# Performance work log

Hardware: AMD Instinct MI355X
Metric: run time of the kernel (lower is better)

## Reference

```python
import jax, jax.numpy as jnp
import numpy as np

B, T, C = 8, 1024, 1024
H, HS = 16, 64            # n_head, head_size
K, STRIDE = 32, 16        # block_length, stride_length
WIN = 128                 # local_window_size
EPS = 1e-5


def _ln(z, w):
    m = jnp.mean(z, axis=-1, keepdims=True)
    v = jnp.var(z, axis=-1, keepdims=True)
    return (z - m) / jnp.sqrt(v + EPS) * w


def setup_inputs() -> dict:
    key = jax.random.key(0)
    ks = jax.random.split(key, 8)
    s = 0.02
    return {
        "x": jax.random.normal(ks[0], (B, T, C), jnp.float32),
        "c_attn_w": jax.random.normal(ks[1], (3 * C, C), jnp.float32) * s,
        "conv_w": jax.random.normal(ks[2], (HS, HS, K), jnp.float32) * s,
        "ln_comp_w": jnp.ones((HS,), jnp.float32),
        "ln_local_w": jnp.ones((C,), jnp.float32),
        "gate_w1": jax.random.normal(ks[3], (C, 2 * C), jnp.float32) * s,
        "gate_ln_w": jnp.ones((C,), jnp.float32),
        "gate_w2": jax.random.normal(ks[4], (2, C), jnp.float32) * s,
        "c_proj_w": jax.random.normal(ks[5], (C, C), jnp.float32) * s,
    }


def reference(x, c_attn_w, conv_w, ln_comp_w, ln_local_w, gate_w1, gate_ln_w, gate_w2, c_proj_w):
    qkv = jnp.einsum('btc,oc->bto', x, c_attn_w)          # [B,T,3C]
    q, k, v = jnp.split(qkv, 3, axis=-1)
    def heads(t):
        return t.reshape(B, T, H, HS).transpose(0, 2, 1, 3)  # [B,H,T,hs]
    q, k, v = heads(q), heads(k), heads(v)

    # CompressionMLP: Conv1d over time + LayerNorm(hs) + exact GELU
    def compress(t):
        xr = t.transpose(0, 1, 3, 2).reshape(B * H, HS, T)   # [B*H, hs, T]
        co = jax.lax.conv_general_dilated(
            xr, conv_w, window_strides=(STRIDE,), padding='VALID',
            dimension_numbers=('NCH', 'OIH', 'NCH'))          # [B*H, hs, NB]
        co = co.transpose(0, 2, 1)                            # [B*H, NB, hs]
        co = jax.nn.gelu(_ln(co, ln_comp_w), approximate=False)
        nb = co.shape[1]
        return co.reshape(B, H, nb, HS)

    kc = compress(k)
    vc = compress(v)
    NB = kc.shape[2]  # 63
    scale = 1.0 / np.sqrt(HS)

    ti = jnp.arange(T)
    band = (ti[None, :] <= ti[:, None]) & (ti[None, :] >= ti[:, None] - WIN)  # [T,T]
    s_loc = jnp.einsum('bhqd,bhkd->bhqk', q, k) * scale
    s_loc = jnp.where(band[None, None], s_loc, -jnp.inf)
    local_out = jnp.einsum('bhqk,bhkd->bhqd', jax.nn.softmax(s_loc, axis=-1), v)
    local_out = local_out.transpose(0, 2, 1, 3).reshape(B, T, C)
    local_norm = _ln(local_out, ln_local_w)

    # compressed-KV attention with block-causal mask: block j <= token i
    bj = jnp.arange(NB)
    cmask = bj[None, :] <= ti[:, None]                        # [T,NB]
    s_cmp = jnp.einsum('bhqd,bhkd->bhqk', q, kc) * scale
    s_cmp = jnp.where(cmask[None, None], s_cmp, -jnp.inf)
    comp_out = jnp.einsum('bhqk,bhkd->bhqd', jax.nn.softmax(s_cmp, axis=-1), vc)
    comp_out = comp_out.transpose(0, 2, 1, 3).reshape(B, T, C)

    # AttentionGating: last-token features -> Linear -> LN -> ReLU -> Linear -> softmax
    feats = jnp.concatenate([local_norm[:, -1, :], comp_out[:, -1, :]], axis=-1)  # [B,2C]
    h = jax.nn.relu(_ln(feats @ gate_w1.T, gate_ln_w))
    gates = jax.nn.softmax(h @ gate_w2.T, axis=-1)            # [B,2]

    combined = gates[:, None, 0:1] * local_norm + gates[:, None, 1:2] * comp_out
    y = jnp.einsum('btc,oc->bto', combined, c_proj_w)
    return y
```

## Files before the change

### kernel.cpp

```cpp
#include <hip/hip_runtime.h>
#include <cstdint>
#include <cmath>
#include <cstddef>

typedef unsigned int u32;
typedef unsigned short u16;
typedef __bf16 bf16x8 __attribute__((ext_vector_type(8)));
typedef float f32x4 __attribute__((ext_vector_type(4)));
typedef u32 u32x4 __attribute__((ext_vector_type(4)));
typedef u32 u32x2 __attribute__((ext_vector_type(2)));

#define DEV static __device__ __forceinline__

DEV float bflo(u32 u) { return __uint_as_float(u << 16); }
DEV float bfhi(u32 u) { return __uint_as_float(u & 0xffff0000u); }
DEV u16 f2bf(float f) {
  u32 u = __float_as_uint(f);
  u += 0x7fffu + ((u >> 16) & 1u);
  return (u16)(u >> 16);
}
DEV f32x4 unpack_bf4(u32x2 r) {
  return (f32x4){bflo(r[0]), bfhi(r[0]), bflo(r[1]), bfhi(r[1])};
}
DEV float wredsum(float v) {
#pragma unroll
  for (int o = 32; o; o >>= 1) v += __shfl_xor(v, o, 64);
  return v;
}

DEV void gload_lds16(const u16* g, u16* lds_base) {
  __builtin_amdgcn_global_load_lds((const __attribute__((address_space(1))) void*)g,
                                   (__attribute__((address_space(3))) void*)lds_base,
                                   16, 0, 0);
}

__global__ __launch_bounds__(256) void fused_cast(const float* __restrict__ x,
                                                  const float* __restrict__ aw,
                                                  const float* __restrict__ pw,
                                                  const float* __restrict__ cw,
                                                  u16* __restrict__ xb,
                                                  u16* __restrict__ wab,
                                                  u16* __restrict__ wpb,
                                                  u16* __restrict__ wcb,
                                                  u16* __restrict__ kcb,
                                                  u16* __restrict__ vcb) {
  const int blk = blockIdx.x;
  if (blk < 12288) {
    const float* src;
    u16* dst;
    int base;
    if (blk < 8192) { src = x; dst = xb; base = blk; }
    else if (blk < 11264) { src = aw; dst = wab; base = blk - 8192; }
    else { src = pw; dst = wpb; base = blk - 11264; }
    const size_t idx = ((size_t)base * 256 + threadIdx.x) * 4;
    const f32x4 v = *(const f32x4*)&src[idx];
    u32x2 r;
    r[0] = (u32)f2bf(v[0]) | ((u32)f2bf(v[1]) << 16);
    r[1] = (u32)f2bf(v[2]) | ((u32)f2bf(v[3]) << 16);
    *(u32x2*)&dst[idx] = r;
  } else if (blk < 12800) {
    const int idx = (blk - 12288) * 256 + threadIdx.x;
    const int o = idx >> 11;
    const int rest = idx & 2047;
    const int i = rest >> 5;
    const int kk = rest & 31;
    wcb[(o << 11) + (kk << 6) + i] = f2bf(cw[idx]);
  } else {
    for (int i = threadIdx.x; i < 8192; i += 256) {
      const int bh = i >> 6, d = i & 63;
      kcb[bh * 4096 + 63 * 64 + d] = 0;
      vcb[bh * 4096 + d * 64 + 63] = 0;
    }
  }
}

template <int OUT_BF16>
__global__ __launch_bounds__(256, 4) void gemm_bt(const u16* __restrict__ A,
                                                  const u16* __restrict__ Bm,
                                                  void* __restrict__ out,
                                                  int M, int N, int K) {
  __shared__ u16 As[128 * 64];
  __shared__ u16 Bs[128 * 64];
  const int tid = threadIdx.x;
  const int lane = tid & 63;
  const int w = tid >> 6;
  const int row0 = blockIdx.x * 128;
  const int col0 = blockIdx.y * 128;
  const int wm = (w >> 1) * 64, wn = (w & 1) * 64;
  const int lr = lane & 15, lq = lane >> 4;
  const int srow = lane >> 3;
  const int scol = ((lane & 7) ^ (srow & 7)) * 8;
  const int pgA = ((lq ^ (lr & 7)) * 8);

  f32x4 acc[4][4] = {};

  for (int k0 = 0; k0 < K; k0 += 64) {
    __syncthreads();
#pragma unroll
    for (int c = 0; c < 4; ++c) {
      const int base_r = w * 32 + c * 8;
      gload_lds16(&A[(size_t)(row0 + base_r + srow) * K + k0 + scol], &As[base_r * 64]);
      gload_lds16(&Bm[(size_t)(col0 + base_r + srow) * K + k0 + scol], &Bs[base_r * 64]);
    }
    __syncthreads();
#pragma unroll
    for (int ks = 0; ks < 2; ++ks) {
      const int pg = pgA ^ (ks << 5);
      bf16x8 af[4], bfr[4];
#pragma unroll
      for (int i = 0; i < 4; ++i) {
        af[i] = *(const bf16x8*)&As[(wm + i * 16 + lr) * 64 + pg];
        bfr[i] = *(const bf16x8*)&Bs[(wn + i * 16 + lr) * 64 + pg];
      }
#pragma unroll
      for (int i = 0; i < 4; ++i)
#pragma unroll
        for (int j = 0; j < 4; ++j)
          acc[i][j] = __builtin_amdgcn_mfma_f32_16x16x32_bf16(af[i], bfr[j], acc[i][j], 0, 0, 0);
    }
  }
#pragma unroll
  for (int i = 0; i < 4; ++i)
#pragma unroll
    for (int j = 0; j < 4; ++j)
#pragma unroll
      for (int rr = 0; rr < 4; ++rr) {
        const int gr = row0 + wm + i * 16 + lq * 4 + rr;
        const int gc = col0 + wn + j * 16 + lr;
        const float v = acc[i][j][rr];
        if (OUT_BF16)
          ((u16*)out)[(size_t)gr * N + gc] = f2bf(v);
        else
          ((float*)out)[(size_t)gr * N + gc] = v;
      }
}

__global__ __launch_bounds__(256) void compress_kernel(const u16* __restrict__ qkv,
                                                       const u16* __restrict__ Wc,
                                                       const float* __restrict__ ln_w,
                                                       u16* __restrict__ kcb,
                                                       u16* __restrict__ vcb) {
  __shared__ u16 As[2][32 * 128];
  __shared__ u16 Bs[2][64 * 128];
  __shared__ float Cs[32][65];
  const int tid = threadIdx.x;
  const int lane = tid & 63, w = tid >> 6;
  const int lr = lane & 15, lq = lane >> 4;
  const int r0 = blockIdx.x * 32;
  const int srcoff = 1024 + (int)blockIdx.y * 1024;

  size_t abase[2];
#pragma unroll
  for (int g2 = 0; g2 < 2; ++g2) {
    const int r = 8 * w + 4 * g2 + (lane >> 4);
    const int gr = r0 + r;
    const int bh = gr / 63;
    const int nb = gr - bh * 63;
    const int b = bh >> 4, h = bh & 15;
    const int jbit = (lane >> 3) & 1;
    const int icol = ((lane & 7) ^ (r & 7)) * 8;
    abase[g2] = (size_t)(b * 1024 + nb * 16 + jbit) * 3072 + srcoff + h * 64 + icol;
  }
  size_t bbase[4];
#pragma unroll
  for (int c = 0; c < 4; ++c) {
    const int rB = 16 * w + 4 * c + (lane >> 4);
    const int Lcol = (((lane & 7) ^ (rB & 7)) | (lane & 8)) * 8;
    bbase[c] = (size_t)rB * 2048 + Lcol;
  }

  auto stage = [&](int it, int bs) {
#pragma unroll
    for (int g2 = 0; g2 < 2; ++g2)
      gload_lds16(&qkv[abase[g2] + (size_t)it * 6144], &As[bs][(8 * w + 4 * g2) * 128]);
#pragma unroll
    for (int c = 0; c < 4; ++c)
      gload_lds16(&Wc[bbase[c] + (size_t)it * 128], &Bs[bs][(16 * w + 4 * c) * 128]);
  };

  const int rw = (w & 1) * 16;
  const int cw = (w >> 1) * 32;
  f32x4 acc[2] = {};

  stage(0, 0);
  for (int it = 0; it < 16; ++it) {
    const int cur = it & 1;
    __syncthreads();
    if (it < 15) stage(it + 1, cur ^ 1);
    const int rowA = rw + lr;
#pragma unroll
    for (int ks = 0; ks < 4; ++ks) {
      const int L = ks * 4 + lq;
      const int pgA = (((L & 7) ^ (rowA & 7)) | (L & 8)) * 8;
      const bf16x8 af = *(const bf16x8*)&As[cur][rowA * 128 + pgA];
#pragma unroll
      for (int j = 0; j < 2; ++j) {
        const int rowB = cw + j * 16 + lr;
        const int pgB = (((L & 7) ^ (rowB & 7)) | (L & 8)) * 8;
        const bf16x8 bfr = *(const bf16x8*)&Bs[cur][rowB * 128 + pgB];
        acc[j] = __builtin_amdgcn_mfma_f32_16x16x32_bf16(af, bfr, acc[j], 0, 0, 0);
      }
    }
  }
  __syncthreads();
#pragma unroll
  for (int j = 0; j < 2; ++j)
#pragma unroll
    for (int rr = 0; rr < 4; ++rr)
      Cs[rw + lq * 4 + rr][cw + j * 16 + lr] = acc[j][rr];
  __syncthreads();
  if (tid < 32) {
    const int gr2 = r0 + tid;
    const int bh2 = gr2 / 63;
    const int nb2 = gr2 - bh2 * 63;
    float s = 0.f, s2 = 0.f;
#pragma unroll 8
    for (int d = 0; d < 64; ++d) {
      const float xv = Cs[tid][d];
      s += xv;
      s2 += xv * xv;
    }
    const float m = s * (1.f / 64.f);
    const float inv = rsqrtf(s2 * (1.f / 64.f) - m * m + 1e-5f);
    if (blockIdx.y == 0) {
      const size_t gb = (size_t)bh2 * 4096 + nb2 * 64;
#pragma unroll 8
      for (int d = 0; d < 64; ++d) {
        const float z = (Cs[tid][d] - m) * inv * ln_w[d];
        kcb[gb + d] = f2bf(0.5f * z * (1.f + erff(z * 0.70710678118f)));
      }
    } else {
      const size_t gb = (size_t)bh2 * 4096 + nb2;
#pragma unroll 8
      for (int d = 0; d < 64; ++d) {
        const float z = (Cs[tid][d] - m) * inv * ln_w[d];
        vcb[gb + d * 64] = f2bf(0.5f * z * (1.f + erff(z * 0.70710678118f)));
      }
    }
  }
}

__global__ __launch_bounds__(256) void attn_fused(const u16* __restrict__ qkv,
                                                  const u16* __restrict__ kcb,
                                                  const u16* __restrict__ vcb,
                                                  u16* __restrict__ loc,
                                                  u16* __restrict__ outc) {
  __shared__ __align__(16) char smem[53248];
  u16* Ks = (u16*)smem;
  u16* Vt = (u16*)smem;
  u16* Ps = (u16*)(smem + 27648);
  const int bh = blockIdx.x;
  const int b = bh >> 4, h = bh & 15;
  const int i0 = blockIdx.y * 64;
  const int jbase = i0 - 128;
  const int tid = threadIdx.x;
  const int lane = tid & 63, w = tid >> 6;
  const int lr = lane & 15, lq = lane >> 4;

  u32x4 vreg[6];
#pragma unroll
  for (int c = 0; c < 6; ++c) {
    const int lin = c * 256 + tid;
    const int s = lin >> 3, d0 = (lin & 7) * 8;
    const int j = jbase + s;
    u32x4 kval = {0, 0, 0, 0}, vval = {0, 0, 0, 0};
    if (j >= 0) {
      const size_t ro = (size_t)(b * 1024 + j) * 3072 + h * 64 + d0;
      kval = *(const u32x4*)&qkv[ro + 1024];
      vval = *(const u32x4*)&qkv[ro + 2048];
    }
    vreg[c] = vval;
    *(u32x4*)&Ks[s * 72 + d0] = kval;
  }
  bf16x8 qf[2];
  {
    const size_t qrow = (size_t)(b * 1024 + i0 + w * 16 + lr) * 3072 + h * 64;
#pragma unroll
    for (int ks = 0; ks < 2; ++ks) qf[ks] = *(const bf16x8*)&qkv[qrow + ks * 32 + lq * 8];
  }
  __syncthreads();

  f32x4 sa[9];
#pragma unroll
  for (int j9 = 0; j9 < 9; ++j9) sa[j9] = (f32x4){0.f, 0.f, 0.f, 0.f};
#pragma unroll
  for (int ks = 0; ks < 2; ++ks)
#pragma unroll
    for (int j9 = 0; j9 < 9; ++j9) {
      const int jt = w + j9;
      const bf16x8 kf = *(const bf16x8*)&Ks[(jt * 16 + lr) * 72 + ks * 32 + lq * 8];
      sa[j9] = __builtin_amdgcn_mfma_f32_16x16x32_bf16(qf[ks], kf, sa[j9], 0, 0, 0);
    }

  const float NINF = -__builtin_inff();
  float mx[4] = {NINF, NINF, NINF, NINF};
#pragma unroll
  for (int j9 = 0; j9 < 9; ++j9) {
    const int s = (w + j9) * 16 + lr;
#pragma unroll
    for (int rr = 0; rr < 4; ++rr) {
      const int qi = w * 16 + lq * 4 + rr;
      const bool valid = (jbase + s >= 0) && (s >= qi) && (s <= qi + 128);
      const float v = valid ? sa[j9][rr] * 0.125f : NINF;
      sa[j9][rr] = v;
      mx[rr] = fmaxf(mx[rr], v);
    }
  }
#pragma unroll
  for (int rr = 0; rr < 4; ++rr)
#pragma unroll
    for (int o = 1; o < 16; o <<= 1) mx[rr] = fmaxf(mx[rr], __shfl_xor(mx[rr], o, 64));
  float sum[4] = {0.f, 0.f, 0.f, 0.f};
#pragma unroll
  for (int j9 = 0; j9 < 9; ++j9)
#pragma unroll
    for (int rr = 0; rr < 4; ++rr) {
      const float p = __expf(sa[j9][rr] - mx[rr]);
      sa[j9][rr] = p;
      sum[rr] += p;
    }
#pragma unroll
  for (int rr = 0; rr < 4; ++rr) {
#pragma unroll
    for (int o = 1; o < 16; o <<= 1) sum[rr] += __shfl_xor(sum[rr], o, 64);
    sum[rr] = 1.0f / sum[rr];
  }
  __syncthreads();

#pragma unroll
  for (int j9 = 0; j9 < 9; ++j9) {
    const int jt = w + j9;
#pragma unroll
    for (int rr = 0; rr < 4; ++rr)
      Ps[(w * 16 + lq * 4 + rr) * 200 + jt * 16 + lr] = f2bf(sa[j9][rr] * sum[rr]);
  }
  {
    const int jz = (w == 0) ? 9 : (w == 1) ? 0 : (w == 2) ? 11 : 2;
#pragma unroll
    for (int rr = 0; rr < 4; ++rr) Ps[(w * 16 + lq * 4 + rr) * 200 + jz * 16 + lr] = 0;
  }
#pragma unroll
  for (int c = 0; c < 6; ++c) {
    const int lin = c * 256 + tid;
    const int s = lin >> 3, d0 = (lin & 7) * 8;
    const u32x4 val = vreg[c];
#pragma unroll
    for (int q = 0; q < 4; ++q) {
      Vt[(d0 + 2 * q) * 200 + s] = (u16)(val[q] & 0xffffu);
      Vt[(d0 + 2 * q + 1) * 200 + s] = (u16)(val[q] >> 16);
    }
  }
  __syncthreads();

  const int W = (w >> 1) * 32;
  f32x4 oa[4];
#pragma unroll
  for (int jt = 0; jt < 4; ++jt) oa[jt] = (f32x4){0.f, 0.f, 0.f, 0.f};
#pragma unroll
  for (int ks = 0; ks < 5; ++ks) {
    const bf16x8 pf = *(const bf16x8*)&Ps[(w * 16 + lr) * 200 + W + ks * 32 + lq * 8];
#pragma unroll
    for (int jt = 0; jt < 4; ++jt) {
      const bf16x8 vf = *(const bf16x8*)&Vt[(jt * 16 + lr) * 200 + W + ks * 32 + lq * 8];
      oa[jt] = __builtin_amdgcn_mfma_f32_16x16x32_bf16(pf, vf, oa[jt], 0, 0, 0);
    }
  }
#pragma unroll
  for (int jt = 0; jt < 4; ++jt)
#pragma unroll
    for (int rr = 0; rr < 4; ++rr)
      loc[(size_t)(b * 1024 + i0 + w * 16 + lq * 4 + rr) * 1024 + h * 64 + jt * 16 + lr] =
          f2bf(oa[jt][rr]);

  __syncthreads();
  u16* Kc = (u16*)smem;
  u16* Vc = (u16*)(smem + 9216);
  u16* Pc = (u16*)(smem + 18432);
  const size_t cb = (size_t)bh * 4096;
  for (int c2 = tid; c2 < 512; c2 += 256) {
    const int nb = c2 >> 3, d0 = (c2 & 7) * 8;
    *(u32x4*)&Kc[nb * 72 + d0] = *(const u32x4*)&kcb[cb + nb * 64 + d0];
  }
  for (int c2 = tid; c2 < 512; c2 += 256) {
    const int d = c2 >> 3, n0 = (c2 & 7) * 8;
    *(u32x4*)&Vc[d * 72 + n0] = *(const u32x4*)&vcb[cb + d * 64 + n0];
  }
  __syncthreads();

  f32x4 ca[4];
#pragma unroll
  for (int j = 0; j < 4; ++j) ca[j] = (f32x4){0.f, 0.f, 0.f, 0.f};
#pragma unroll
  for (int ks = 0; ks < 2; ++ks)
#pragma unroll
    for (int j = 0; j < 4; ++j) {
      const bf16x8 kf = *(const bf16x8*)&Kc[(j * 16 + lr) * 72 + ks * 32 + lq * 8];
      ca[j] = __builtin_amdgcn_mfma_f32_16x16x32_bf16(qf[ks], kf, ca[j], 0, 0, 0);
    }
  float mc[4] = {NINF, NINF, NINF, NINF};
#pragma unroll
  for (int j = 0; j < 4; ++j) {
    const int s = j * 16 + lr;
#pragma unroll
    for (int rr = 0; rr < 4; ++rr) {
      const int i = i0 + w * 16 + lq * 4 + rr;
      const bool valid = (s <= i) && (s < 63);
      const float v = valid ? ca[j][rr] * 0.125f : NINF;
      ca[j][rr] = v;
      mc[rr] = fmaxf(mc[rr], v);
    }
  }
#pragma unroll
  for (int rr = 0; rr < 4; ++rr)
#pragma unroll
    for (int o = 1; o < 16; o <<= 1) mc[rr] = fmaxf(mc[rr], __shfl_xor(mc[rr], o, 64));
  float sc[4] = {0.f, 0.f, 0.f, 0.f};
#pragma unroll
  for (int j = 0; j < 4; ++j)
#pragma unroll
    for (int rr = 0; rr < 4; ++rr) {
      const float p = __expf(ca[j][rr] - mc[rr]);
      ca[j][rr] = p;
      sc[rr] += p;
    }
#pragma unroll
  for (int rr = 0; rr < 4; ++rr) {
#pragma unroll
    for (int o = 1; o < 16; o <<= 1) sc[rr] += __shfl_xor(sc[rr], o, 64);
    sc[rr] = 1.0f / sc[rr];
  }
#pragma unroll
  for (int j = 0; j < 4; ++j)
#pragma unroll
    for (int rr = 0; rr < 4; ++rr)
      Pc[(w * 16 + lq * 4 + rr) * 72 + j * 16 + lr] = f2bf(ca[j][rr] * sc[rr]);
  __syncthreads();

  f32x4 co[4];
#pragma unroll
  for (int jt = 0; jt < 4; ++jt) co[jt] = (f32x4){0.f, 0.f, 0.f, 0.f};
#pragma unroll
  for (int ks = 0; ks < 2; ++ks) {
    const bf16x8 pf = *(const bf16x8*)&Pc[(w * 16 + lr) * 72 + ks * 32 + lq * 8];
#pragma unroll
    for (int jt = 0; jt < 4; ++jt) {
      const bf16x8 vf = *(const bf16x8*)&Vc[(jt * 16 + lr) * 72 + ks * 32 + lq * 8];
      co[jt] = __builtin_amdgcn_mfma_f32_16x16x32_bf16(pf, vf, co[jt], 0, 0, 0);
    }
  }
#pragma unroll
  for (int jt = 0; jt < 4; ++jt)
#pragma unroll
    for (int rr = 0; rr < 4; ++rr)
      outc[(size_t)(b * 1024 + i0 + w * 16 + lq * 4 + rr) * 1024 + h * 64 + jt * 16 + lr] =
          f2bf(co[jt][rr]);
}

__global__ __launch_bounds__(256) void ln_feats(const u16* __restrict__ locb,
                                                const u16* __restrict__ compb,
                                                const float* __restrict__ lnw,
                                                float* __restrict__ feats) {
  const int b = blockIdx.x, tid = threadIdx.x;
  const size_t base = ((size_t)b * 1024 + 1023) * 1024 + tid * 4;
  const f32x4 v = unpack_bf4(*(const u32x2*)&locb[base]);
  float s = v[0] + v[1] + v[2] + v[3];
  float s2 = v[0] * v[0] + v[1] * v[1] + v[2] * v[2] + v[3] * v[3];
  s = wredsum(s);
  s2 = wredsum(s2);
  __shared__ float rs[4], rs2[4];
  const int w = tid >> 6, lane = tid & 63;
  if (!lane) { rs[w] = s; rs2[w] = s2; }
  __syncthreads();
  s = rs[0] + rs[1] + rs[2] + rs[3];
  s2 = rs2[0] + rs2[1] + rs2[2] + rs2[3];
  const float m = s * (1.f / 1024.f);
  const float inv = rsqrtf(s2 * (1.f / 1024.f) - m * m + 1e-5f);
  const f32x4 wv = *(const f32x4*)&lnw[tid * 4];
  f32x4 o;
#pragma unroll
  for (int k = 0; k < 4; ++k) o[k] = (v[k] - m) * inv * wv[k];
  *(f32x4*)&feats[b * 2048 + tid * 4] = o;
  *(f32x4*)&feats[b * 2048 + 1024 + tid * 4] = unpack_bf4(*(const u32x2*)&compb[base]);
}

__global__ __launch_bounds__(256) void gate_gemv(const float* __restrict__ feats,
                                                 const float* __restrict__ w1,
                                                 float* __restrict__ hraw) {
  const int o = blockIdx.x * 4 + (threadIdx.x >> 6);
  const int lane = threadIdx.x & 63;
  const float* wr = &w1[(size_t)o * 2048];
  float acc[8] = {};
#pragma unroll
  for (int it = 0; it < 8; ++it) {
    const int c = (it * 64 + lane) * 4;
    const f32x4 wv = *(const f32x4*)&wr[c];
#pragma unroll
    for (int b = 0; b < 8; ++b) {
      const f32x4 fv = *(const f32x4*)&feats[b * 2048 + c];
      acc[b] += fv[0] * wv[0] + fv[1] * wv[1] + fv[2] * wv[2] + fv[3] * wv[3];
    }
  }
#pragma unroll
  for (int b = 0; b < 8; ++b) acc[b] = wredsum(acc[b]);
  if (lane == 0) {
#pragma unroll
    for (int b = 0; b < 8; ++b) hraw[b * 1024 + o] = acc[b];
  }
}

__global__ __launch_bounds__(256) void gate_fin(const float* __restrict__ hraw,
                                                const float* __restrict__ lnw,
                                                const float* __restrict__ w2,
                                                float* __restrict__ gates) {
  const int b = blockIdx.x, tid = threadIdx.x;
  const f32x4 v = *(const f32x4*)&hraw[(size_t)b * 1024 + tid * 4];
  float s = v[0] + v[1] + v[2] + v[3];
  float s2 = v[0] * v[0] + v[1] * v[1] + v[2] * v[2] + v[3] * v[3];
  s = wredsum(s);
  s2 = wredsum(s2);
  __shared__ float rs[4], rs2[4];
  const int w = tid >> 6, lane = tid & 63;
  if (!lane) { rs[w] = s; rs2[w] = s2; }
  __syncthreads();
  s = rs[0] + rs[1] + rs[2] + rs[3];
  s2 = rs2[0] + rs2[1] + rs2[2] + rs2[3];
  const float m = s * (1.f / 1024.f);
  const float inv = rsqrtf(s2 * (1.f / 1024.f) - m * m + 1e-5f);
  float p0 = 0.f, p1 = 0.f;
#pragma unroll
  for (int k = 0; k < 4; ++k) {
    float hh = (v[k] - m) * inv * lnw[tid * 4 + k];
    hh = fmaxf(hh, 0.f);
    p0 += hh * w2[tid * 4 + k];
    p1 += hh * w2[1024 + tid * 4 + k];
  }
  p0 = wredsum(p0);
  p1 = wredsum(p1);
  __syncthreads();
  if (!lane) { rs[w] = p0; rs2[w] = p1; }
  __syncthreads();
  if (tid == 0) {
    const float l0 = rs[0] + rs[1] + rs[2] + rs[3];
    const float l1 = rs2[0] + rs2[1] + rs2[2] + rs2[3];
    const float mm = fmaxf(l0, l1);
    const float e0 = __expf(l0 - mm), e1 = __expf(l1 - mm);
    const float iv = 1.f / (e0 + e1);
    gates[b * 2] = e0 * iv;
    gates[b * 2 + 1] = e1 * iv;
  }
}

__global__ __launch_bounds__(256) void combine_ln_cast(const u16* __restrict__ locb,
                                                       const u16* __restrict__ compb,
                                                       const float* __restrict__ lnw,
                                                       const float* __restrict__ gates,
                                                       u16* __restrict__ outb) {
  const int row = blockIdx.x, tid = threadIdx.x;
  const size_t base = (size_t)row * 1024 + tid * 4;
  const f32x4 v = unpack_bf4(*(const u32x2*)&locb[base]);
  float s = v[0] + v[1] + v[2] + v[3];
  float s2 = v[0] * v[0] + v[1] * v[1] + v[2] * v[2] + v[3] * v[3];
  s = wredsum(s);
  s2 = wredsum(s2);
  __shared__ float rs[4], rs2[4];
  const int w = tid >> 6, lane = tid & 63;
  if (!lane) { rs[w] = s; rs2[w] = s2; }
  __syncthreads();
  s = rs[0] + rs[1] + rs[2] + rs[3];
  s2 = rs2[0] + rs2[1] + rs2[2] + rs2[3];
  const float m = s * (1.f / 1024.f);
  const float inv = rsqrtf(s2 * (1.f / 1024.f) - m * m + 1e-5f);
  const int b = row >> 10;
  const float g0 = gates[2 * b], g1 = gates[2 * b + 1];
  const f32x4 wv = *(const f32x4*)&lnw[tid * 4];
  const f32x4 c = unpack_bf4(*(const u32x2*)&compb[base]);
  float ov[4];
#pragma unroll
  for (int k = 0; k < 4; ++k) ov[k] = g0 * ((v[k] - m) * inv * wv[k]) + g1 * c[k];
  u32x2 r;
  r[0] = (u32)f2bf(ov[0]) | ((u32)f2bf(ov[1]) << 16);
  r[1] = (u32)f2bf(ov[2]) | ((u32)f2bf(ov[3]) << 16);
  *(u32x2*)&outb[base] = r;
}

extern "C" void kernel_launch(void* const* d_in, const int* in_sizes, int n_in,
                              void* d_out, int out_size, void* d_ws, size_t ws_size,
                              hipStream_t stream) {
  const float* x = (const float*)d_in[0];
  const float* c_attn_w = (const float*)d_in[1];
  const float* conv_w = (const float*)d_in[2];
  const float* ln_comp_w = (const float*)d_in[3];
  const float* ln_local_w = (const float*)d_in[4];
  const float* gate_w1 = (const float*)d_in[5];
  const float* gate_ln_w = (const float*)d_in[6];
  const float* gate_w2 = (const float*)d_in[7];
  const float* c_proj_w = (const float*)d_in[8];
  float* y = (float*)d_out;

  char* ws = (char*)d_ws;
  size_t off = 0;
  auto alloc = [&](size_t bytes) -> void* {
    void* p = ws + off;
    off += (bytes + 255) & ~(size_t)255;
    return p;
  };
  u16* qkvb = (u16*)alloc((size_t)8192 * 3072 * 2);
  u16* xb = (u16*)alloc((size_t)8192 * 1024 * 2);
  u16* wab = (u16*)alloc((size_t)3072 * 1024 * 2);
  u16* wpb = (u16*)alloc((size_t)1024 * 1024 * 2);
  u16* wcb = (u16*)alloc((size_t)64 * 2048 * 2);
  u16* kcb = (u16*)alloc((size_t)128 * 4096 * 2);
  u16* vcb = (u16*)alloc((size_t)128 * 4096 * 2);
  u16* locb = (u16*)alloc((size_t)8192 * 1024 * 2);
  u16* compb = (u16*)alloc((size_t)8192 * 1024 * 2);
  float* feats = (float*)alloc((size_t)8 * 2048 * 4);
  float* hraw = (float*)alloc((size_t)8192 * 4);
  float* gates = (float*)alloc(64);
  u16* combb = (u16*)alloc((size_t)8192 * 1024 * 2);

  fused_cast<<<12801, 256, 0, stream>>>(x, c_attn_w, c_proj_w, conv_w, xb, wab, wpb, wcb, kcb,
                                        vcb);

  gemm_bt<1><<<dim3(64, 24), 256, 0, stream>>>(xb, wab, qkvb, 8192, 3072, 1024);

  compress_kernel<<<dim3(252, 2), 256, 0, stream>>>(qkvb, wcb, ln_comp_w, kcb, vcb);

  attn_fused<<<dim3(128, 16), 256, 0, stream>>>(qkvb, kcb, vcb, locb, compb);

  ln_feats<<<8, 256, 0, stream>>>(locb, compb, ln_local_w, feats);
  gate_gemv<<<256, 256, 0, stream>>>(feats, gate_w1, hraw);
  gate_fin<<<8, 256, 0, stream>>>(hraw, gate_ln_w, gate_w2, gates);

  combine_ln_cast<<<8192, 256, 0, stream>>>(locb, compb, ln_local_w, gates, combb);

  gemm_bt<0><<<dim3(64, 8), 256, 0, stream>>>(combb, wpb, y, 8192, 1024, 1024);
}
```

Measured before the change: 274.0 us.

## Shrink attn_fused LDS via split V-transpose passes, XOR swizzle, early compressed-KV prefetch

Shared memory for the fused attention kernel drops from 53 KB to about 40 KB. V is transposed into LDS in two halves of the head dimension, one before and one after the first half of the P·V MMA, and stored with an XOR swizzle to avoid bank conflicts. The compressed K/V loads are issued into registers at kernel start, and launch bounds ask for 4 blocks per CU. This aims at higher occupancy and hidden global latency, at the cost of extra barriers and register pressure.

```diff
diff --git a/kernel.cpp b/kernel.cpp
--- a/kernel.cpp
+++ b/kernel.cpp
@@ -240,15 +240,18 @@
   }
 }
 
-__global__ __launch_bounds__(256) void attn_fused(const u16* __restrict__ qkv,
-                                                  const u16* __restrict__ kcb,
-                                                  const u16* __restrict__ vcb,
-                                                  u16* __restrict__ loc,
-                                                  u16* __restrict__ outc) {
-  __shared__ __align__(16) char smem[53248];
+__global__ __launch_bounds__(256, 4) void attn_fused(const u16* __restrict__ qkv,
+                                                     const u16* __restrict__ kcb,
+                                                     const u16* __restrict__ vcb,
+                                                     u16* __restrict__ loc,
+                                                     u16* __restrict__ outc) {
+  __shared__ __align__(16) char smem[40448];
   u16* Ks = (u16*)smem;
-  u16* Vt = (u16*)smem;
-  u16* Ps = (u16*)(smem + 27648);
+  u16* Ps = (u16*)smem;
+  u16* Vt = (u16*)(smem + 27648);
+  u16* Kc = (u16*)smem;
+  u16* Vc = (u16*)(smem + 9216);
+  u16* Pc = (u16*)(smem + 18432);
   const int bh = blockIdx.x;
   const int b = bh >> 4, h = bh & 15;
   const int i0 = blockIdx.y * 64;
@@ -256,6 +259,8 @@
   const int tid = threadIdx.x;
   const int lane = tid & 63, w = tid >> 6;
   const int lr = lane & 15, lq = lane >> 4;
+  const int j3 = lane & 3;
+  const int dh1 = (lane >> 2) & 1;
 
   u32x4 vreg[6];
 #pragma unroll
@@ -272,11 +277,34 @@
     vreg[c] = vval;
     *(u32x4*)&Ks[s * 72 + d0] = kval;
   }
+  if (!dh1) {
+    const int d0 = (lane & 7) * 8;
+#pragma unroll
+    for (int c = 0; c < 6; ++c) {
+      const int s = (c * 256 + tid) >> 3;
+      const int sc = (((s >> 3) ^ j3) << 3) + (s & 7);
+      const u32x4 val = vreg[c];
+#pragma unroll
+      for (int q = 0; q < 4; ++q) {
+        Vt[(d0 + 2 * q) * 200 + sc] = (u16)(val[q] & 0xffffu);
+        Vt[(d0 + 2 * q + 1) * 200 + sc] = (u16)(val[q] >> 16);
+      }
+    }
+  }
   bf16x8 qf[2];
   {
     const size_t qrow = (size_t)(b * 1024 + i0 + w * 16 + lr) * 3072 + h * 64;
 #pragma unroll
     for (int ks = 0; ks < 2; ++ks) qf[ks] = *(const bf16x8*)&qkv[qrow + ks * 32 + lq * 8];
+  }
+  const size_t cb = (size_t)bh * 4096;
+  u32x4 kcreg[2], vcreg[2];
+#pragma unroll
+  for (int c2 = 0; c2 < 2; ++c2) {
+    const int i2 = c2 * 256 + tid;
+    const size_t o2 = (size_t)(i2 >> 3) * 64 + (i2 & 7) * 8;
+    kcreg[c2] = *(const u32x4*)&kcb[cb + o2];
+    vcreg[c2] = *(const u32x4*)&vcb[cb + o2];
   }
   __syncthreads();
 
@@ -339,20 +367,10 @@
 #pragma unroll
     for (int rr = 0; rr < 4; ++rr) Ps[(w * 16 + lq * 4 + rr) * 200 + jz * 16 + lr] = 0;
   }
-#pragma unroll
-  for (int c = 0; c < 6; ++c) {
-    const int lin = c * 256 + tid;
-    const int s = lin >> 3, d0 = (lin & 7) * 8;
-    const u32x4 val = vreg[c];
-#pragma unroll
-    for (int q = 0; q < 4; ++q) {
-      Vt[(d0 + 2 * q) * 200 + s] = (u16)(val[q] & 0xffffu);
-      Vt[(d0 + 2 * q + 1) * 200 + s] = (u16)(val[q] >> 16);
-    }
-  }
   __syncthreads();
 
   const int W = (w >> 1) * 32;
+  const int G0 = W >> 3;
   f32x4 oa[4];
 #pragma unroll
   for (int jt = 0; jt < 4; ++jt) oa[jt] = (f32x4){0.f, 0.f, 0.f, 0.f};
@@ -360,30 +378,62 @@
   for (int ks = 0; ks < 5; ++ks) {
     const bf16x8 pf = *(const bf16x8*)&Ps[(w * 16 + lr) * 200 + W + ks * 32 + lq * 8];
 #pragma unroll
-    for (int jt = 0; jt < 4; ++jt) {
-      const bf16x8 vf = *(const bf16x8*)&Vt[(jt * 16 + lr) * 200 + W + ks * 32 + lq * 8];
-      oa[jt] = __builtin_amdgcn_mfma_f32_16x16x32_bf16(pf, vf, oa[jt], 0, 0, 0);
-    }
-  }
-#pragma unroll
-  for (int jt = 0; jt < 4; ++jt)
+    for (int jl = 0; jl < 2; ++jl) {
+      const int rl = jl * 16 + lr;
+      const int g = G0 + ks * 4 + lq;
+      const bf16x8 vf = *(const bf16x8*)&Vt[rl * 200 + ((g ^ (rl >> 3)) << 3)];
+      oa[jl] = __builtin_amdgcn_mfma_f32_16x16x32_bf16(pf, vf, oa[jl], 0, 0, 0);
+    }
+  }
+#pragma unroll
+  for (int jt = 0; jt < 2; ++jt)
 #pragma unroll
     for (int rr = 0; rr < 4; ++rr)
       loc[(size_t)(b * 1024 + i0 + w * 16 + lq * 4 + rr) * 1024 + h * 64 + jt * 16 + lr] =
           f2bf(oa[jt][rr]);
-
-  __syncthreads();
-  u16* Kc = (u16*)smem;
-  u16* Vc = (u16*)(smem + 9216);
-  u16* Pc = (u16*)(smem + 18432);
-  const size_t cb = (size_t)bh * 4096;
-  for (int c2 = tid; c2 < 512; c2 += 256) {
-    const int nb = c2 >> 3, d0 = (c2 & 7) * 8;
-    *(u32x4*)&Kc[nb * 72 + d0] = *(const u32x4*)&kcb[cb + nb * 64 + d0];
-  }
-  for (int c2 = tid; c2 < 512; c2 += 256) {
-    const int d = c2 >> 3, n0 = (c2 & 7) * 8;
-    *(u32x4*)&Vc[d * 72 + n0] = *(const u32x4*)&vcb[cb + d * 64 + n0];
+  __syncthreads();
+
+  if (dh1) {
+    const int d0 = (lane & 7) * 8 - 32;
+#pragma unroll
+    for (int c = 0; c < 6; ++c) {
+      const int s = (c * 256 + tid) >> 3;
+      const int sc = (((s >> 3) ^ j3) << 3) + (s & 7);
+      const u32x4 val = vreg[c];
+#pragma unroll
+      for (int q = 0; q < 4; ++q) {
+        Vt[(d0 + 2 * q) * 200 + sc] = (u16)(val[q] & 0xffffu);
+        Vt[(d0 + 2 * q + 1) * 200 + sc] = (u16)(val[q] >> 16);
+      }
+    }
+  }
+  __syncthreads();
+
+#pragma unroll
+  for (int ks = 0; ks < 5; ++ks) {
+    const bf16x8 pf = *(const bf16x8*)&Ps[(w * 16 + lr) * 200 + W + ks * 32 + lq * 8];
+#pragma unroll
+    for (int jl = 0; jl < 2; ++jl) {
+      const int rl = jl * 16 + lr;
+      const int g = G0 + ks * 4 + lq;
+      const bf16x8 vf = *(const bf16x8*)&Vt[rl * 200 + ((g ^ (rl >> 3)) << 3)];
+      oa[2 + jl] = __builtin_amdgcn_mfma_f32_16x16x32_bf16(pf, vf, oa[2 + jl], 0, 0, 0);
+    }
+  }
+#pragma unroll
+  for (int jt = 2; jt < 4; ++jt)
+#pragma unroll
+    for (int rr = 0; rr < 4; ++rr)
+      loc[(size_t)(b * 1024 + i0 + w * 16 + lq * 4 + rr) * 1024 + h * 64 + jt * 16 + lr] =
+          f2bf(oa[jt][rr]);
+
+  __syncthreads();
+#pragma unroll
+  for (int c2 = 0; c2 < 2; ++c2) {
+    const int i2 = c2 * 256 + tid;
+    const int r2 = i2 >> 3, o2 = (i2 & 7) * 8;
+    *(u32x4*)&Kc[r2 * 72 + o2] = kcreg[c2];
+    *(u32x4*)&Vc[r2 * 72 + o2] = vcreg[c2];
   }
   __syncthreads();
 
```

New measurement: 288.1 us. +5.1%, slower.
